# Kernel optimization log

Hardware: AMD Instinct MI355X
Metric: run time of the kernel (lower is better)

Reference implementation:

```python
import jax, jax.numpy as jnp
import numpy as np

DIM = 1024
HEADS = 16
HEAD_DIM = DIM // HEADS  # 64
EPS = 1e-5


def layer_norm(x, w, b):
    # LayerNorm over last dim (head_dim), matching nn.LayerNorm defaults
    mu = jnp.mean(x, axis=-1, keepdims=True)
    var = jnp.mean(jnp.square(x - mu), axis=-1, keepdims=True)
    return (x - mu) * jax.lax.rsqrt(var + EPS) * w + b


def apply_rotary_emb(x, freqs):
    # x: [B, S, H, D]; freqs: [S, D/2] angles. Interleaved (complex) rotary:
    # pairs (x[2i], x[2i+1]) rotated by angle freqs[:, i].
    x1 = x[..., 0::2]
    x2 = x[..., 1::2]
    cos = jnp.cos(freqs)[None, :, None, :]
    sin = jnp.sin(freqs)[None, :, None, :]
    r1 = x1 * cos - x2 * sin
    r2 = x1 * sin + x2 * cos
    return jnp.stack([r1, r2], axis=-1).reshape(x.shape)


def setup_inputs() -> dict:
    key = jax.random.key(0)
    ks = jax.random.split(key, 8)
    B, S = 2, 2048
    x = jax.random.normal(ks[0], (B, S, DIM), dtype=jnp.float32)
    freqs = jax.random.uniform(ks[1], (S, HEAD_DIM // 2), dtype=jnp.float32)
    sc = 1.0 / np.sqrt(DIM)
    w_qkv = jax.random.normal(ks[2], (DIM, 4 * DIM), dtype=jnp.float32) * sc
    w_out = jax.random.normal(ks[3], (DIM, DIM), dtype=jnp.float32) * sc
    qn_w = jnp.ones((HEAD_DIM,), jnp.float32)
    qn_b = jnp.zeros((HEAD_DIM,), jnp.float32)
    kn_w = jnp.ones((HEAD_DIM,), jnp.float32)
    kn_b = jnp.zeros((HEAD_DIM,), jnp.float32)
    return {"x": x, "freqs": freqs, "w_qkv": w_qkv, "w_out": w_out,
            "qn_w": qn_w, "qn_b": qn_b, "kn_w": kn_w, "kn_b": kn_b}


def reference(x, freqs, w_qkv, w_out, qn_w, qn_b, kn_w, kn_b):
    B, S, _ = x.shape
    qkv = x @ w_qkv  # [B, S, 4*DIM]
    q, k, v, gate = jnp.split(qkv, 4, axis=-1)
    q = q.reshape(B, S, HEADS, HEAD_DIM)
    k = k.reshape(B, S, HEADS, HEAD_DIM)
    v = v.reshape(B, S, HEADS, HEAD_DIM)
    q = layer_norm(q, qn_w, qn_b)
    k = layer_norm(k, kn_w, kn_b)
    q = apply_rotary_emb(q, freqs)
    k = apply_rotary_emb(k, freqs)
    # flash_attn_func: non-causal softmax attention, scale 1/sqrt(head_dim)
    scale = 1.0 / np.sqrt(HEAD_DIM)
    scores = jnp.einsum('bqhd,bkhd->bhqk', q, k) * scale
    probs = jax.nn.softmax(scores, axis=-1)
    o = jnp.einsum('bhqk,bkhd->bqhd', probs, v)
    o = o.reshape(B, S, DIM)
    o = o * jax.nn.sigmoid(gate)
    return o @ w_out
```

## Files before the change

kernel.cpp:

```cpp
#include <hip/hip_runtime.h>


typedef _Float16 f16;
typedef _Float16 f16x8 __attribute__((ext_vector_type(8)));
typedef _Float16 f16x4 __attribute__((ext_vector_type(4)));
typedef float    f32x4 __attribute__((ext_vector_type(4)));

#define MFMA16(a, b, c) __builtin_amdgcn_mfma_f32_16x16x32_f16((a), (b), (c), 0, 0, 0)

__device__ __forceinline__ void gload16(const void* g, void* l) {
  __builtin_amdgcn_global_load_lds(
      (const __attribute__((address_space(1))) void*)g,
      (__attribute__((address_space(3))) void*)l, 16, 0, 0);
}

__device__ __forceinline__ float exp2_fast(float x) {
#if __has_builtin(__builtin_amdgcn_exp2f)
  return __builtin_amdgcn_exp2f(x);
#else
  float r;
  asm("v_exp_f32 %0, %1" : "=v"(r) : "v"(x));
  return r;
#endif
}
__device__ __forceinline__ unsigned pkrtz(float a, float b) {
  typedef __fp16 hf16x2 __attribute__((ext_vector_type(2)));
  union { hf16x2 h; unsigned u; } c;
  c.h = __builtin_amdgcn_cvt_pkrtz(a, b);
  return c.u;
}

__global__ void rope_table_kernel(const float* __restrict__ freqs, float* __restrict__ tbl) {
  int i = blockIdx.x * 256 + threadIdx.x;
  if (i >= 2048 * 32) return;
  int s = i >> 5, j = i & 31;
  float f = freqs[i];
  tbl[s * 64 + j]      = cosf(f);
  tbl[s * 64 + 32 + j] = sinf(f);
}

__global__ void cast_f16_kernel(const float* __restrict__ in, f16* __restrict__ out, int n8) {
  int i = blockIdx.x * 256 + threadIdx.x;
  if (i >= n8) return;
  float4 a = ((const float4*)in)[2 * i];
  float4 b = ((const float4*)in)[2 * i + 1];
  f16x8 o;
  o[0] = (f16)a.x; o[1] = (f16)a.y; o[2] = (f16)a.z; o[3] = (f16)a.w;
  o[4] = (f16)b.x; o[5] = (f16)b.y; o[6] = (f16)b.z; o[7] = (f16)b.w;
  ((f16x8*)out)[i] = o;
}

__global__ void transpose_cast_kernel(const float* __restrict__ in, f16* __restrict__ out,
                                      int R, int C) {
  __shared__ float t[64][65];
  int c0 = blockIdx.x * 64, r0 = blockIdx.y * 64;
  int tx = threadIdx.x & 15, ty = threadIdx.x >> 4;
#pragma unroll
  for (int i = 0; i < 4; ++i) {
    float4 v = *(const float4*)&in[(size_t)(r0 + ty + 16 * i) * C + c0 + tx * 4];
    t[ty + 16 * i][tx * 4 + 0] = v.x;
    t[ty + 16 * i][tx * 4 + 1] = v.y;
    t[ty + 16 * i][tx * 4 + 2] = v.z;
    t[ty + 16 * i][tx * 4 + 3] = v.w;
  }
  __syncthreads();
#pragma unroll
  for (int i = 0; i < 4; ++i) {
    int n = c0 + ty + 16 * i;
    int k = r0 + tx * 4;
    f16x4 o;
    o[0] = (f16)t[tx * 4 + 0][ty + 16 * i];
    o[1] = (f16)t[tx * 4 + 1][ty + 16 * i];
    o[2] = (f16)t[tx * 4 + 2][ty + 16 * i];
    o[3] = (f16)t[tx * 4 + 3][ty + 16 * i];
    *(f16x4*)&out[(size_t)n * R + k] = o;
  }
}

__global__ void fill_debug_kernel(float* out, int n) {
  int i = blockIdx.x * 256 + threadIdx.x;
  if (i < n) out[i] = 12345.0f;
}

template <int EPI>
__global__ __launch_bounds__(256, 2) void gemm_f16(
    const f16* __restrict__ A, const f16* __restrict__ B,
    float* __restrict__ Cout, int M, int N, int K,
    float* __restrict__ q_f32, float* __restrict__ k_f32,
    float* __restrict__ gate_f32, f16* __restrict__ v_t) {
  __shared__ f16 sA[2][128 * 64], sB[2][128 * 64];
  const int tid = threadIdx.x, lane = tid & 63;
  const int wave = tid >> 6, wm = wave >> 1, wn = wave & 1;
  const int lg = lane >> 4, lr = lane & 15;
  const int n0 = blockIdx.x * 128, m0 = blockIdx.y * 128;

  auto stg = [&](int k0, int p) {
#pragma unroll
    for (int r = 0; r < 4; ++r) {
      int off = (tid + r * 256) * 16;
      int row = off >> 7;
      int col = ((off & 127) ^ ((row & 7) << 4)) >> 1;
      gload16(A + (size_t)(m0 + row) * K + k0 + col, (char*)sA[p] + off);
      gload16(B + (size_t)(n0 + row) * K + k0 + col, (char*)sB[p] + off);
    }
  };

  f32x4 acc[4][4];
#pragma unroll
  for (int m = 0; m < 4; ++m)
#pragma unroll
    for (int n = 0; n < 4; ++n) acc[m][n] = (f32x4){0.f, 0.f, 0.f, 0.f};

  stg(0, 0);
  const int NT = K >> 6;
  int cur = 0;
  for (int t = 0; t < NT; ++t, cur ^= 1) {
    __syncthreads();
    if (t + 1 < NT) stg((t + 1) << 6, cur ^ 1);
#pragma unroll
    for (int ks = 0; ks < 2; ++ks) {
      f16x8 bfr[4];
#pragma unroll
      for (int n = 0; n < 4; ++n) {
        int row = wn * 64 + n * 16 + lr;
        int boff = (row << 7) + (ks << 6) + (lg << 4);
        boff ^= (row & 7) << 4;
        bfr[n] = *(const f16x8*)((const char*)sB[cur] + boff);
      }
#pragma unroll
      for (int m = 0; m < 4; ++m) {
        int row = wm * 64 + m * 16 + lr;
        int aoff = (row << 7) + (ks << 6) + (lg << 4);
        aoff ^= (row & 7) << 4;
        f16x8 afr = *(const f16x8*)((const char*)sA[cur] + aoff);
#pragma unroll
        for (int n = 0; n < 4; ++n) acc[m][n] = MFMA16(afr, bfr[n], acc[m][n]);
      }
    }
  }

  if (EPI == 0) {
#pragma unroll
    for (int m = 0; m < 4; ++m) {
      int row = m0 + wm * 64 + m * 16 + 4 * lg;
#pragma unroll
      for (int n = 0; n < 4; ++n) {
        int col = n0 + wn * 64 + n * 16 + lr;
#pragma unroll
        for (int r = 0; r < 4; ++r) Cout[(size_t)(row + r) * N + col] = acc[m][n][r];
      }
    }
  } else {
    int region = n0 >> 10;
#pragma unroll
    for (int m = 0; m < 4; ++m) {
      int row = m0 + wm * 64 + m * 16 + 4 * lg;
#pragma unroll
      for (int n = 0; n < 4; ++n) {
        int col = n0 + wn * 64 + n * 16 + lr;
        if (region == 0) {
#pragma unroll
          for (int r = 0; r < 4; ++r) q_f32[(size_t)(row + r) * 1024 + col] = acc[m][n][r];
        } else if (region == 1) {
#pragma unroll
          for (int r = 0; r < 4; ++r) k_f32[(size_t)(row + r) * 1024 + col - 1024] = acc[m][n][r];
        } else if (region == 3) {
#pragma unroll
          for (int r = 0; r < 4; ++r) gate_f32[(size_t)(row + r) * 1024 + col - 3072] = acc[m][n][r];
        } else {
          int c = col - 2048, hh = c >> 6, d = c & 63;
          int b = row >> 11, s = row & 2047;
          f16x4 pv;
          pv[0] = (f16)acc[m][n][0];
          pv[1] = (f16)acc[m][n][1];
          pv[2] = (f16)acc[m][n][2];
          pv[3] = (f16)acc[m][n][3];
          *(f16x4*)&v_t[(size_t)((b * 16 + hh) * 64 + d) * 2048 + s] = pv;
        }
      }
    }
  }
}

__global__ void norm_rope_kernel(const float* __restrict__ qf, const float* __restrict__ kf,
                                 const float* __restrict__ tbl,
                                 const float* __restrict__ qn_w, const float* __restrict__ qn_b,
                                 const float* __restrict__ kn_w, const float* __restrict__ kn_b,
                                 f16* __restrict__ q_h, f16* __restrict__ k_h) {
  int row = blockIdx.x;
  int s = row & 2047;
  int hh = threadIdx.x >> 4, sub = threadIdx.x & 15;
  int base = row * 1024 + hh * 64 + sub * 4;
  float c0 = tbl[s * 64 + sub * 2 + 0], c1 = tbl[s * 64 + sub * 2 + 1];
  float s0 = tbl[s * 64 + 32 + sub * 2 + 0], s1 = tbl[s * 64 + 32 + sub * 2 + 1];
#pragma unroll
  for (int which = 0; which < 2; ++which) {
    const float* src = which ? kf : qf;
    const float* wp = which ? kn_w : qn_w;
    const float* bp = which ? kn_b : qn_b;
    f16* dst = which ? k_h : q_h;
    float4 x = *(const float4*)&src[base];
    float sum = x.x + x.y + x.z + x.w;
    sum += __shfl_xor(sum, 1); sum += __shfl_xor(sum, 2);
    sum += __shfl_xor(sum, 4); sum += __shfl_xor(sum, 8);
    float mu = sum * (1.0f / 64.0f);
    float d0 = x.x - mu, d1 = x.y - mu, d2 = x.z - mu, d3 = x.w - mu;
    float sq = d0 * d0 + d1 * d1 + d2 * d2 + d3 * d3;
    sq += __shfl_xor(sq, 1); sq += __shfl_xor(sq, 2);
    sq += __shfl_xor(sq, 4); sq += __shfl_xor(sq, 8);
    float rstd = rsqrtf(sq * (1.0f / 64.0f) + 1e-5f);
    float4 w = *(const float4*)&wp[sub * 4];
    float4 bb = *(const float4*)&bp[sub * 4];
    float n0 = d0 * rstd * w.x + bb.x;
    float n1 = d1 * rstd * w.y + bb.y;
    float n2 = d2 * rstd * w.z + bb.z;
    float n3 = d3 * rstd * w.w + bb.w;
    float r0 = n0 * c0 - n1 * s0, r1 = n0 * s0 + n1 * c0;
    float r2 = n2 * c1 - n3 * s1, r3 = n2 * s1 + n3 * c1;
    f16x4 ov;
    ov[0] = (f16)r0; ov[1] = (f16)r1; ov[2] = (f16)r2; ov[3] = (f16)r3;
    *(f16x4*)&dst[base] = ov;
  }
}

__global__ __launch_bounds__(256, 2) void attn_kernel(const f16* __restrict__ q_h,
                                                      const f16* __restrict__ k_h,
                                                      const f16* __restrict__ v_t,
                                                      const float* __restrict__ gate_f32,
                                                      f16* __restrict__ a16) {
  __shared__ __align__(16) char smem[65536];
  const int tid = threadIdx.x, lane = tid & 63, wave = tid >> 6;
  const int lg = lane >> 4, lr = lane & 15;
  const int bh = blockIdx.x >> 4, qt = blockIdx.x & 15;
  const int b = bh >> 4, h = bh & 15;
  const int qrow0 = b * 2048 + qt * 128 + wave * 32;

  auto stage = [&](int kv0, int p) {
    char* kb = smem + p * 16384;
    char* vb = smem + 32768 + p * 16384;
#pragma unroll
    for (int r = 0; r < 4; ++r) {
      int off = (tid + r * 256) * 16;
      {
        int row = off >> 7;
        int col = ((off & 127) ^ ((row & 7) << 4)) >> 1;
        int g = ((row >> 5) << 5) + (((row >> 2) & 3) << 3) + (((row >> 4) & 1) << 2) + (row & 3);
        gload16(&k_h[(size_t)(b * 2048 + kv0 + g) * 1024 + h * 64 + col], kb + off);
      }
      {
        int d = off >> 8;
        int col = ((off & 255) ^ ((d & 15) << 4)) >> 1;
        gload16(&v_t[(size_t)(bh * 64 + d) * 2048 + kv0 + col], vb + off);
      }
    }
  };

  f16x8 qf[2][2];
#pragma unroll
  for (int n = 0; n < 2; ++n)
#pragma unroll
    for (int ks = 0; ks < 2; ++ks)
      qf[n][ks] = *(const f16x8*)&q_h[(size_t)(qrow0 + n * 16 + lr) * 1024 + h * 64 + ks * 32 + lg * 8];

  f16x8 ones;
#pragma unroll
  for (int j = 0; j < 8; ++j) ones[j] = (f16)1.0f;

  f32x4 accO[4][2];
#pragma unroll
  for (int m = 0; m < 4; ++m) {
    accO[m][0] = (f32x4){0.f, 0.f, 0.f, 0.f};
    accO[m][1] = (f32x4){0.f, 0.f, 0.f, 0.f};
  }
  f32x4 accL[2] = {(f32x4){0.f, 0.f, 0.f, 0.f}, (f32x4){0.f, 0.f, 0.f, 0.f}};
  float mrun[2] = {-1e30f, -1e30f};
  const float SCL2 = 0.125f * 1.44269504f;
  const float THRP = 44.36f;
  const f32x4 fz = (f32x4){0.f, 0.f, 0.f, 0.f};

  stage(0, 0);

  int cur = 0;
  for (int t = 0; t < 16; ++t, cur ^= 1) {
    __syncthreads();
    if (t < 15) stage((t + 1) * 128, cur ^ 1);

    const char* kb = smem + cur * 16384;
    const char* vb = smem + 32768 + cur * 16384;

    f32x4 st[8][2];
    __builtin_amdgcn_s_setprio(1);
#pragma unroll
    for (int m = 0; m < 8; ++m) {
      int row = m * 16 + lr;
      int koff0 = ((row << 7) + (lg << 4)) ^ ((row & 7) << 4);
      int koff1 = ((row << 7) + 64 + (lg << 4)) ^ ((row & 7) << 4);
      f16x8 a0 = *(const f16x8*)(kb + koff0);
      f16x8 a1 = *(const f16x8*)(kb + koff1);
      st[m][0] = MFMA16(a1, qf[0][1], MFMA16(a0, qf[0][0], fz));
      st[m][1] = MFMA16(a1, qf[1][1], MFMA16(a0, qf[1][0], fz));
    }
    __builtin_amdgcn_s_setprio(0);

    uint2 pdw[2][8];
#pragma unroll
    for (int n = 0; n < 2; ++n) {
      float t03 = fmaxf(fmaxf(fmaxf(st[0][n][0], st[0][n][1]), fmaxf(st[0][n][2], st[0][n][3])),
                        fmaxf(fmaxf(st[1][n][0], st[1][n][1]), fmaxf(st[1][n][2], st[1][n][3])));
      float t47 = fmaxf(fmaxf(fmaxf(st[2][n][0], st[2][n][1]), fmaxf(st[2][n][2], st[2][n][3])),
                        fmaxf(fmaxf(st[3][n][0], st[3][n][1]), fmaxf(st[3][n][2], st[3][n][3])));
      float t8b = fmaxf(fmaxf(fmaxf(st[4][n][0], st[4][n][1]), fmaxf(st[4][n][2], st[4][n][3])),
                        fmaxf(fmaxf(st[5][n][0], st[5][n][1]), fmaxf(st[5][n][2], st[5][n][3])));
      float tcf = fmaxf(fmaxf(fmaxf(st[6][n][0], st[6][n][1]), fmaxf(st[6][n][2], st[6][n][3])),
                        fmaxf(fmaxf(st[7][n][0], st[7][n][1]), fmaxf(st[7][n][2], st[7][n][3])));
      float vm = fmaxf(fmaxf(t03, t47), fmaxf(t8b, tcf));
      vm = fmaxf(vm, __shfl_xor(vm, 16));
      vm = fmaxf(vm, __shfl_xor(vm, 32));
      if (__any(vm > mrun[n] + THRP)) {
        float mnew = fmaxf(mrun[n], vm);
        float fac = exp2_fast((mrun[n] - mnew) * SCL2);
        mrun[n] = mnew;
        accL[n] *= fac;
#pragma unroll
        for (int m = 0; m < 4; ++m) accO[m][n] *= fac;
      }
      float mc = mrun[n] * SCL2;
#pragma unroll
      for (int m = 0; m < 8; ++m) {
        float p0 = exp2_fast(st[m][n][0] * SCL2 - mc);
        float p1 = exp2_fast(st[m][n][1] * SCL2 - mc);
        float p2 = exp2_fast(st[m][n][2] * SCL2 - mc);
        float p3 = exp2_fast(st[m][n][3] * SCL2 - mc);
        pdw[n][m].x = pkrtz(p0, p1);
        pdw[n][m].y = pkrtz(p2, p3);
      }
    }

    f16x8 pb[2][4];
#pragma unroll
    for (int n = 0; n < 2; ++n)
#pragma unroll
      for (int ks = 0; ks < 4; ++ks) {
        union { uint4 u; f16x8 h; } c;
        c.u = make_uint4(pdw[n][2 * ks].x, pdw[n][2 * ks].y,
                         pdw[n][2 * ks + 1].x, pdw[n][2 * ks + 1].y);
        pb[n][ks] = c.h;
      }
    __builtin_amdgcn_s_setprio(1);
#pragma unroll
    for (int m = 0; m < 4; ++m)
#pragma unroll
      for (int ks = 0; ks < 4; ++ks) {
        int d = m * 16 + lr;
        int voff = (d << 8) + (ks << 6) + (lg << 4);
        voff ^= (d & 15) << 4;
        f16x8 av = *(const f16x8*)(vb + voff);
        accO[m][0] = MFMA16(av, pb[0][ks], accO[m][0]);
        accO[m][1] = MFMA16(av, pb[1][ks], accO[m][1]);
      }
#pragma unroll
    for (int ks = 0; ks < 4; ++ks) {
      accL[0] = MFMA16(ones, pb[0][ks], accL[0]);
      accL[1] = MFMA16(ones, pb[1][ks], accL[1]);
    }
    __builtin_amdgcn_s_setprio(0);
  }

#pragma unroll
  for (int n = 0; n < 2; ++n) {
    float rl = 1.0f / accL[n][0];
    int orow = qrow0 + n * 16 + lr;
#pragma unroll
    for (int m = 0; m < 4; ++m) {
      size_t idx = (size_t)orow * 1024 + h * 64 + m * 16 + lg * 4;
      float4 gv = *(const float4*)&gate_f32[idx];
      f16x4 ov;
      ov[0] = (f16)(accO[m][n][0] * rl / (1.f + __expf(-gv.x)));
      ov[1] = (f16)(accO[m][n][1] * rl / (1.f + __expf(-gv.y)));
      ov[2] = (f16)(accO[m][n][2] * rl / (1.f + __expf(-gv.z)));
      ov[3] = (f16)(accO[m][n][3] * rl / (1.f + __expf(-gv.w)));
      *(f16x4*)&a16[idx] = ov;
    }
  }
}

extern "C" void kernel_launch(void* const* d_in, const int* in_sizes, int n_in,
                              void* d_out, int out_size, void* d_ws, size_t ws_size,
                              hipStream_t stream) {
  const float* x      = (const float*)d_in[0];
  const float* freqs  = (const float*)d_in[1];
  const float* w_qkv  = (const float*)d_in[2];
  const float* w_out  = (const float*)d_in[3];
  const float* qn_w   = (const float*)d_in[4];
  const float* qn_b   = (const float*)d_in[5];
  const float* kn_w   = (const float*)d_in[6];
  const float* kn_b   = (const float*)d_in[7];
  float* out = (float*)d_out;
  char* ws = (char*)d_ws;
  const size_t MB = 1024 * 1024;
  float* q_f32    = (float*)(ws + 0);
  float* k_f32    = (float*)(ws + 16 * MB);
  float* gate_f32 = (float*)(ws + 32 * MB);
  f16*   v_t      = (f16*)(ws + 48 * MB);
  f16*   x16      = (f16*)(ws + 56 * MB);
  f16*   wq16     = (f16*)(ws + 64 * MB);
  f16*   wo16     = (f16*)(ws + 72 * MB);
  f16*   q_h      = (f16*)(ws + 74 * MB);
  f16*   k_h      = (f16*)(ws + 82 * MB);
  float* tbl      = (float*)(ws + 90 * MB);
  f16*   a16      = x16;

  if (ws_size < (size_t)91 * MB) {
    fill_debug_kernel<<<(out_size + 255) / 256, 256, 0, stream>>>(out, out_size);
    return;
  }

  rope_table_kernel<<<256, 256, 0, stream>>>(freqs, tbl);
  cast_f16_kernel<<<2048, 256, 0, stream>>>(x, x16, 524288);
  transpose_cast_kernel<<<dim3(64, 16), 256, 0, stream>>>(w_qkv, wq16, 1024, 4096);
  transpose_cast_kernel<<<dim3(16, 16), 256, 0, stream>>>(w_out, wo16, 1024, 1024);

  gemm_f16<1><<<dim3(32, 32), 256, 0, stream>>>(x16, wq16, nullptr, 4096, 4096, 1024,
                                                q_f32, k_f32, gate_f32, v_t);
  norm_rope_kernel<<<4096, 256, 0, stream>>>(q_f32, k_f32, tbl, qn_w, qn_b, kn_w, kn_b, q_h, k_h);
  attn_kernel<<<512, 256, 0, stream>>>(q_h, k_h, v_t, gate_f32, a16);
  gemm_f16<0><<<dim3(8, 32), 256, 0, stream>>>(a16, wo16, out, 4096, 1024, 1024,
                                               nullptr, nullptr, nullptr, nullptr);
}
```

Before: 150.6 us.

## Fuse head LayerNorm, RoPE and gate sigmoid into QKV GEMM epilogue

The QKV GEMM epilogue now applies per-head LayerNorm and interleaved rotary embedding directly to the q and k accumulator tiles, writing fp16 q_h and k_h. This removes the separate norm_rope kernel and the fp32 q and k round trip through memory. The gate sigmoid is also computed in the epilogue and stored as fp16, so attention reads half the bytes and skips the exp. The cost is a heavier GEMM epilogue with cross-lane shuffles and scattered 2-byte stores.

```diff
diff --git a/kernel.cpp b/kernel.cpp
--- a/kernel.cpp
+++ b/kernel.cpp
@@ -86,8 +86,11 @@
 __global__ __launch_bounds__(256, 2) void gemm_f16(
     const f16* __restrict__ A, const f16* __restrict__ B,
     float* __restrict__ Cout, int M, int N, int K,
-    float* __restrict__ q_f32, float* __restrict__ k_f32,
-    float* __restrict__ gate_f32, f16* __restrict__ v_t) {
+    const float* __restrict__ qn_w, const float* __restrict__ qn_b,
+    const float* __restrict__ kn_w, const float* __restrict__ kn_b,
+    const float* __restrict__ tbl,
+    f16* __restrict__ q_h, f16* __restrict__ k_h,
+    f16* __restrict__ g16, f16* __restrict__ v_t) {
   __shared__ f16 sA[2][128 * 64], sB[2][128 * 64];
   const int tid = threadIdx.x, lane = tid & 63;
   const int wave = tid >> 6, wm = wave >> 1, wn = wave & 1;
@@ -151,82 +154,88 @@
       }
     }
   } else {
-    int region = n0 >> 10;
-#pragma unroll
-    for (int m = 0; m < 4; ++m) {
-      int row = m0 + wm * 64 + m * 16 + 4 * lg;
-#pragma unroll
-      for (int n = 0; n < 4; ++n) {
-        int col = n0 + wn * 64 + n * 16 + lr;
-        if (region == 0) {
-#pragma unroll
-          for (int r = 0; r < 4; ++r) q_f32[(size_t)(row + r) * 1024 + col] = acc[m][n][r];
-        } else if (region == 1) {
-#pragma unroll
-          for (int r = 0; r < 4; ++r) k_f32[(size_t)(row + r) * 1024 + col - 1024] = acc[m][n][r];
-        } else if (region == 3) {
-#pragma unroll
-          for (int r = 0; r < 4; ++r) gate_f32[(size_t)(row + r) * 1024 + col - 3072] = acc[m][n][r];
-        } else {
+    const int region = n0 >> 10;
+    if (region == 2) {
+#pragma unroll
+      for (int m = 0; m < 4; ++m) {
+        int row = m0 + wm * 64 + m * 16 + 4 * lg;
+#pragma unroll
+        for (int n = 0; n < 4; ++n) {
+          int col = n0 + wn * 64 + n * 16 + lr;
           int c = col - 2048, hh = c >> 6, d = c & 63;
-          int b = row >> 11, s = row & 2047;
+          int bb = row >> 11, s = row & 2047;
           f16x4 pv;
           pv[0] = (f16)acc[m][n][0];
           pv[1] = (f16)acc[m][n][1];
           pv[2] = (f16)acc[m][n][2];
           pv[3] = (f16)acc[m][n][3];
-          *(f16x4*)&v_t[(size_t)((b * 16 + hh) * 64 + d) * 2048 + s] = pv;
+          *(f16x4*)&v_t[(size_t)((bb * 16 + hh) * 64 + d) * 2048 + s] = pv;
         }
       }
-    }
-  }
-}
-
-__global__ void norm_rope_kernel(const float* __restrict__ qf, const float* __restrict__ kf,
-                                 const float* __restrict__ tbl,
-                                 const float* __restrict__ qn_w, const float* __restrict__ qn_b,
-                                 const float* __restrict__ kn_w, const float* __restrict__ kn_b,
-                                 f16* __restrict__ q_h, f16* __restrict__ k_h) {
-  int row = blockIdx.x;
-  int s = row & 2047;
-  int hh = threadIdx.x >> 4, sub = threadIdx.x & 15;
-  int base = row * 1024 + hh * 64 + sub * 4;
-  float c0 = tbl[s * 64 + sub * 2 + 0], c1 = tbl[s * 64 + sub * 2 + 1];
-  float s0 = tbl[s * 64 + 32 + sub * 2 + 0], s1 = tbl[s * 64 + 32 + sub * 2 + 1];
-#pragma unroll
-  for (int which = 0; which < 2; ++which) {
-    const float* src = which ? kf : qf;
-    const float* wp = which ? kn_w : qn_w;
-    const float* bp = which ? kn_b : qn_b;
-    f16* dst = which ? k_h : q_h;
-    float4 x = *(const float4*)&src[base];
-    float sum = x.x + x.y + x.z + x.w;
-    sum += __shfl_xor(sum, 1); sum += __shfl_xor(sum, 2);
-    sum += __shfl_xor(sum, 4); sum += __shfl_xor(sum, 8);
-    float mu = sum * (1.0f / 64.0f);
-    float d0 = x.x - mu, d1 = x.y - mu, d2 = x.z - mu, d3 = x.w - mu;
-    float sq = d0 * d0 + d1 * d1 + d2 * d2 + d3 * d3;
-    sq += __shfl_xor(sq, 1); sq += __shfl_xor(sq, 2);
-    sq += __shfl_xor(sq, 4); sq += __shfl_xor(sq, 8);
-    float rstd = rsqrtf(sq * (1.0f / 64.0f) + 1e-5f);
-    float4 w = *(const float4*)&wp[sub * 4];
-    float4 bb = *(const float4*)&bp[sub * 4];
-    float n0 = d0 * rstd * w.x + bb.x;
-    float n1 = d1 * rstd * w.y + bb.y;
-    float n2 = d2 * rstd * w.z + bb.z;
-    float n3 = d3 * rstd * w.w + bb.w;
-    float r0 = n0 * c0 - n1 * s0, r1 = n0 * s0 + n1 * c0;
-    float r2 = n2 * c1 - n3 * s1, r3 = n2 * s1 + n3 * c1;
-    f16x4 ov;
-    ov[0] = (f16)r0; ov[1] = (f16)r1; ov[2] = (f16)r2; ov[3] = (f16)r3;
-    *(f16x4*)&dst[base] = ov;
+    } else if (region == 3) {
+#pragma unroll
+      for (int m = 0; m < 4; ++m) {
+        int row = m0 + wm * 64 + m * 16 + 4 * lg;
+#pragma unroll
+        for (int n = 0; n < 4; ++n) {
+          int col = n0 + wn * 64 + n * 16 + lr - 3072;
+#pragma unroll
+          for (int r = 0; r < 4; ++r) {
+            float sg = 1.0f / (1.0f + exp2_fast(acc[m][n][r] * -1.44269504f));
+            g16[(size_t)(row + r) * 1024 + col] = (f16)sg;
+          }
+        }
+      }
+    } else {
+      const float* wln = region ? kn_w : qn_w;
+      const float* bln = region ? kn_b : qn_b;
+      f16* dst = region ? k_h : q_h;
+      const int colbase = (n0 & 1023) + wn * 64;
+      float wv[4], bv[4];
+#pragma unroll
+      for (int n = 0; n < 4; ++n) {
+        wv[n] = wln[n * 16 + lr];
+        bv[n] = bln[n * 16 + lr];
+      }
+      const float sgn = (lr & 1) ? 1.0f : -1.0f;
+#pragma unroll
+      for (int m = 0; m < 4; ++m) {
+        int row0 = m0 + wm * 64 + m * 16 + 4 * lg;
+#pragma unroll
+        for (int r = 0; r < 4; ++r) {
+          int row = row0 + r;
+          float sum = acc[m][0][r] + acc[m][1][r] + acc[m][2][r] + acc[m][3][r];
+          sum += __shfl_xor(sum, 1); sum += __shfl_xor(sum, 2);
+          sum += __shfl_xor(sum, 4); sum += __shfl_xor(sum, 8);
+          float mu = sum * (1.0f / 64.0f);
+          float dv0 = acc[m][0][r] - mu, dv1 = acc[m][1][r] - mu;
+          float dv2 = acc[m][2][r] - mu, dv3 = acc[m][3][r] - mu;
+          float sq = dv0 * dv0 + dv1 * dv1 + dv2 * dv2 + dv3 * dv3;
+          sq += __shfl_xor(sq, 1); sq += __shfl_xor(sq, 2);
+          sq += __shfl_xor(sq, 4); sq += __shfl_xor(sq, 8);
+          float rstd = rsqrtf(sq * (1.0f / 64.0f) + 1e-5f);
+          int s = row & 2047;
+          const float* tb = tbl + s * 64;
+          float dvs[4] = {dv0, dv1, dv2, dv3};
+#pragma unroll
+          for (int n = 0; n < 4; ++n) {
+            float y = dvs[n] * rstd * wv[n] + bv[n];
+            float yp = __shfl_xor(y, 1);
+            int j = (n * 16 + lr) >> 1;
+            float cs = tb[j], si = tb[32 + j];
+            float o = y * cs + sgn * (yp * si);
+            dst[(size_t)row * 1024 + colbase + n * 16 + lr] = (f16)o;
+          }
+        }
+      }
+    }
   }
 }
 
 __global__ __launch_bounds__(256, 2) void attn_kernel(const f16* __restrict__ q_h,
                                                       const f16* __restrict__ k_h,
                                                       const f16* __restrict__ v_t,
-                                                      const float* __restrict__ gate_f32,
+                                                      const f16* __restrict__ g16,
                                                       f16* __restrict__ a16) {
   __shared__ __align__(16) char smem[65536];
   const int tid = threadIdx.x, lane = tid & 63, wave = tid >> 6;
@@ -373,12 +382,12 @@
 #pragma unroll
     for (int m = 0; m < 4; ++m) {
       size_t idx = (size_t)orow * 1024 + h * 64 + m * 16 + lg * 4;
-      float4 gv = *(const float4*)&gate_f32[idx];
+      f16x4 gv = *(const f16x4*)&g16[idx];
       f16x4 ov;
-      ov[0] = (f16)(accO[m][n][0] * rl / (1.f + __expf(-gv.x)));
-      ov[1] = (f16)(accO[m][n][1] * rl / (1.f + __expf(-gv.y)));
-      ov[2] = (f16)(accO[m][n][2] * rl / (1.f + __expf(-gv.z)));
-      ov[3] = (f16)(accO[m][n][3] * rl / (1.f + __expf(-gv.w)));
+      ov[0] = (f16)(accO[m][n][0] * rl * (float)gv[0]);
+      ov[1] = (f16)(accO[m][n][1] * rl * (float)gv[1]);
+      ov[2] = (f16)(accO[m][n][2] * rl * (float)gv[2]);
+      ov[3] = (f16)(accO[m][n][3] * rl * (float)gv[3]);
       *(f16x4*)&a16[idx] = ov;
     }
   }
@@ -398,19 +407,17 @@
   float* out = (float*)d_out;
   char* ws = (char*)d_ws;
   const size_t MB = 1024 * 1024;
-  float* q_f32    = (float*)(ws + 0);
-  float* k_f32    = (float*)(ws + 16 * MB);
-  float* gate_f32 = (float*)(ws + 32 * MB);
-  f16*   v_t      = (f16*)(ws + 48 * MB);
-  f16*   x16      = (f16*)(ws + 56 * MB);
-  f16*   wq16     = (f16*)(ws + 64 * MB);
-  f16*   wo16     = (f16*)(ws + 72 * MB);
-  f16*   q_h      = (f16*)(ws + 74 * MB);
-  f16*   k_h      = (f16*)(ws + 82 * MB);
-  float* tbl      = (float*)(ws + 90 * MB);
-  f16*   a16      = x16;
-
-  if (ws_size < (size_t)91 * MB) {
+  f16*   v_t   = (f16*)(ws + 0);
+  f16*   x16   = (f16*)(ws + 8 * MB);
+  f16*   wq16  = (f16*)(ws + 16 * MB);
+  f16*   wo16  = (f16*)(ws + 24 * MB);
+  f16*   q_h   = (f16*)(ws + 26 * MB);
+  f16*   k_h   = (f16*)(ws + 34 * MB);
+  f16*   g16   = (f16*)(ws + 42 * MB);
+  float* tbl   = (float*)(ws + 50 * MB);
+  f16*   a16   = x16;
+
+  if (ws_size < (size_t)51 * MB) {
     fill_debug_kernel<<<(out_size + 255) / 256, 256, 0, stream>>>(out, out_size);
     return;
   }
@@ -421,9 +428,10 @@
   transpose_cast_kernel<<<dim3(16, 16), 256, 0, stream>>>(w_out, wo16, 1024, 1024);
 
   gemm_f16<1><<<dim3(32, 32), 256, 0, stream>>>(x16, wq16, nullptr, 4096, 4096, 1024,
-                                                q_f32, k_f32, gate_f32, v_t);
-  norm_rope_kernel<<<4096, 256, 0, stream>>>(q_f32, k_f32, tbl, qn_w, qn_b, kn_w, kn_b, q_h, k_h);
-  attn_kernel<<<512, 256, 0, stream>>>(q_h, k_h, v_t, gate_f32, a16);
+                                                qn_w, qn_b, kn_w, kn_b, tbl,
+                                                q_h, k_h, g16, v_t);
+  attn_kernel<<<512, 256, 0, stream>>>(q_h, k_h, v_t, g16, a16);
   gemm_f16<0><<<dim3(8, 32), 256, 0, stream>>>(a16, wo16, out, 4096, 1024, 1024,
+                                               nullptr, nullptr, nullptr, nullptr, nullptr,
                                                nullptr, nullptr, nullptr, nullptr);
 }
```

New measurement: 147.4 us. 2.1% less time.
